# Kernel tuning notes

Measured on AMD Instinct MI355X. Metric: run time of the kernel, lower is better.

## Reference

```python
import jax, jax.numpy as jnp
import numpy as np


def setup_inputs() -> dict:
    key = jax.random.key(0)
    k1, k2, k3 = jax.random.split(key, 3)
    B, S, D, H = 64, 512, 512, 1024
    # xavier_uniform bounds
    def xavier(k, shape):
        fan_in, fan_out = shape
        limit = float(np.sqrt(6.0 / (fan_in + fan_out)))
        return jax.random.uniform(k, shape, jnp.float32, -limit, limit)
    x = jax.random.normal(k1, (B, S, D), dtype=jnp.float32)
    weight_ih = xavier(k2, (D, 4 * H))
    weight_hh = xavier(k3, (H, 4 * H))
    bias = jnp.zeros((4 * H,), dtype=jnp.float32)
    return {"x": x, "weight_ih": weight_ih, "weight_hh": weight_hh, "bias": bias}


def reference(x, weight_ih, weight_hh, bias):
    # x: (B, S, D). Faithful to the per-step loop: gates = x_t@W_ih + h@W_hh + b,
    # gate order [i, f, g, o]; zero initial states broadcast over batch.
    B = x.shape[0]
    HS = weight_hh.shape[0]
    h0 = jnp.zeros((B, HS), dtype=x.dtype)
    c0 = jnp.zeros((B, HS), dtype=x.dtype)

    def step(carry, x_t):
        h, c = carry
        gates = x_t @ weight_ih + h @ weight_hh + bias  # (B, 4*HS)
        i_t = jax.nn.sigmoid(gates[:, :HS])
        f_t = jax.nn.sigmoid(gates[:, HS:2 * HS])
        g_t = jnp.tanh(gates[:, 2 * HS:3 * HS])
        o_t = jax.nn.sigmoid(gates[:, 3 * HS:])
        c_new = f_t * c + i_t * g_t
        h_new = o_t * jnp.tanh(c_new)
        return (h_new, c_new), h_new

    xs = jnp.swapaxes(x, 0, 1)  # (S, B, D) for scan over time
    (h_t, c_t), hs = jax.lax.scan(step, (h0, c0), xs)
    hidden_seq = jnp.swapaxes(hs, 0, 1)  # (B, S, HS)
    return hidden_seq, h_t, c_t
```

## Files before the change

### kernel.cpp

```cpp
#include <hip/hip_runtime.h>
#include <hip/hip_bf16.h>

typedef __attribute__((ext_vector_type(8))) short bf16x8;
typedef __attribute__((ext_vector_type(4))) float f32x4;

constexpr int NB = 64, NS = 512, ND = 512, NH = 1024;
constexpr int G4H = 4096;
constexpr int NWG = 256, NTHR = 512;
constexpr int PS  = 20;
constexpr int TRB = 3072;

__device__ inline unsigned short f2bf(float f) {
  union { float f; unsigned u; } v; v.f = f;
  unsigned r = v.u + 0x7FFFu + ((v.u >> 16) & 1u);
  return (unsigned short)(r >> 16);
}
__device__ inline float sigmoidf_fast(float x) { return 1.0f / (1.0f + __expf(-x)); }
__device__ inline float tanhf_fast(float x) {
  float e = __expf(2.0f * x);
  return 1.0f - 2.0f / (e + 1.0f);
}
__device__ inline int swz(int row, int off) { return row * TRB + (off ^ ((row & 7) << 4)); }

__global__ void prep_kernel(const float* __restrict__ x,
                            unsigned short* __restrict__ xbf,
                            unsigned short* __restrict__ hbuf) {
  const int idx = blockIdx.x * blockDim.x + threadIdx.x;
  const int nthr = gridDim.x * blockDim.x;
  const int nh4 = NB * NH * 2 / 16;
  uint4* h4 = (uint4*)hbuf;
  for (int i = idx; i < nh4; i += nthr) h4[i] = uint4{0, 0, 0, 0};
  for (int i = idx; i < nh4; i += nthr)
    h4[nh4 + i] = uint4{0x00010001u, 0x00010001u, 0x00010001u, 0x00010001u};
  const float4* x4 = (const float4*)x;
  ushort4* xo = (ushort4*)xbf;
  const int n4 = NB * NS * ND / 4;
  for (int i = idx; i < n4; i += nthr) {
    float4 v = x4[i];
    ushort4 o;
    o.x = f2bf(v.x); o.y = f2bf(v.y); o.z = f2bf(v.z); o.w = f2bf(v.w);
    xo[i] = o;
  }
}

__global__ __launch_bounds__(NTHR)
void lstm_kernel(const float* __restrict__ Wih,
                 const float* __restrict__ Whh,
                 const float* __restrict__ bias,
                 const unsigned short* __restrict__ xbf,
                 unsigned short* __restrict__ hbuf,
                 float* __restrict__ out)
{
  const int tid  = threadIdx.x;
  const int wg   = blockIdx.x;
  const int wave = tid >> 6;
  const int lane = tid & 63;
  const int bb   = wg >> 6;
  const int hb   = wg & 63;
  const int gp   = wave & 1;
  const int q    = wave >> 1;

  __shared__ unsigned short tile[16 * 1536];
  __shared__ float part[16][16 * PS];
  __shared__ float c_state[256];

  if (tid < 256) c_state[tid] = 0.0f;

  const int kg0  = (lane >> 4) << 3;
  const int colb = (hb << 4) + (lane & 15);
  bf16x8 wx[2][4], wh[2][8];
#pragma unroll
  for (int gg = 0; gg < 2; ++gg) {
    const int col = ((gp * 2 + gg) << 10) + colb;
#pragma unroll
    for (int s = 0; s < 4; ++s) {
      const int k0 = (q * 4 + s) * 32 + kg0;
#pragma unroll
      for (int j = 0; j < 8; ++j)
        wx[gg][s][j] = (short)f2bf(Wih[(size_t)(k0 + j) * G4H + col]);
    }
#pragma unroll
    for (int u = 0; u < 8; ++u) {
      const int k0 = (q * 8 + u) * 32 + kg0;
#pragma unroll
      for (int j = 0; j < 8; ++j)
        wh[gg][u][j] = (short)f2bf(Whh[(size_t)(k0 + j) * G4H + col]);
    }
  }

  for (int c = tid; c < 1024; c += NTHR) {
    const int row = c >> 6, sl = c & 63;
    const unsigned short* src = xbf + (size_t)(bb * 16 + row) * (NS * ND) + sl * 8;
    *(uint4*)((char*)tile + swz(row, sl * 16)) = *(const uint4*)src;
  }
  for (int c = tid; c < 2048; c += NTHR) {
    const int row = c >> 7, sl = c & 127;
    *(uint4*)((char*)tile + swz(row, 1024 + sl * 16)) = uint4{0, 0, 0, 0};
  }
  __syncthreads();

  const int arow = lane & 15;
  float* ht_out = out + (size_t)NB * NS * NH;
  float* ct_out = ht_out + NB * NH;

  for (int t = 0; t < NS; ++t) {
    constexpr unsigned long long M = 0x0000000100000001ull;
    const unsigned long long T = ((t >> 1) & 1) ? M : 0ull;
    unsigned long long hq0[4], hq1[4];
    const unsigned long long* hp[4];
    if (t > 0) {
      const unsigned short* hbase = hbuf + (size_t)(t & 1) * (NB * NH);
#pragma unroll
      for (int u = 0; u < 4; ++u) {
        const int row = 2 * wave + (u >> 1);
        const int sl  = (u & 1) * 64 + lane;
        hp[u] = (const unsigned long long*)(hbase + (size_t)(bb * 16 + row) * NH + sl * 8);
        hq0[u] = __hip_atomic_load(hp[u],     __ATOMIC_RELAXED, __HIP_MEMORY_SCOPE_AGENT);
        hq1[u] = __hip_atomic_load(hp[u] + 1, __ATOMIC_RELAXED, __HIP_MEMORY_SCOPE_AGENT);
      }
    }

    f32x4 a0 = {0.f, 0.f, 0.f, 0.f}, a1 = {0.f, 0.f, 0.f, 0.f};
#pragma unroll
    for (int s = 0; s < 4; ++s) {
      const int off = ((q * 4 + s) * 32 + kg0) * 2;
      bf16x8 af = *(const bf16x8*)((const char*)tile + swz(arow, off));
      a0 = __builtin_amdgcn_mfma_f32_16x16x32_bf16(af, wx[0][s], a0, 0, 0, 0);
      a1 = __builtin_amdgcn_mfma_f32_16x16x32_bf16(af, wx[1][s], a1, 0, 0, 0);
    }

    if (t > 0) {
      while (true) {
        int stale = 0;
#pragma unroll
        for (int u = 0; u < 4; ++u)
          if ((((hq0[u] ^ T) | (hq1[u] ^ T)) & M) != 0ull) stale |= (1 << u);
        if (__all(stale == 0)) break;
#pragma unroll
        for (int u = 0; u < 4; ++u)
          if (stale & (1 << u)) {
            hq0[u] = __hip_atomic_load(hp[u],     __ATOMIC_RELAXED, __HIP_MEMORY_SCOPE_AGENT);
            hq1[u] = __hip_atomic_load(hp[u] + 1, __ATOMIC_RELAXED, __HIP_MEMORY_SCOPE_AGENT);
          }
      }
#pragma unroll
      for (int u = 0; u < 4; ++u) {
        const int row = 2 * wave + (u >> 1);
        const int sl  = (u & 1) * 64 + lane;
        uint4 v;
        v.x = (unsigned int)hq0[u];
        v.y = (unsigned int)(hq0[u] >> 32);
        v.z = (unsigned int)hq1[u];
        v.w = (unsigned int)(hq1[u] >> 32);
        *(uint4*)((char*)tile + swz(row, 1024 + sl * 16)) = v;
      }
    }
    __syncthreads();

#pragma unroll
    for (int u = 0; u < 8; ++u) {
      const int off = 1024 + ((q * 8 + u) * 32 + kg0) * 2;
      bf16x8 af = *(const bf16x8*)((const char*)tile + swz(arow, off));
      a0 = __builtin_amdgcn_mfma_f32_16x16x32_bf16(af, wh[0][u], a0, 0, 0, 0);
      a1 = __builtin_amdgcn_mfma_f32_16x16x32_bf16(af, wh[1][u], a1, 0, 0, 0);
    }

    {
      const int r0 = (lane >> 4) << 2;
      const int cc = lane & 15;
#pragma unroll
      for (int j = 0; j < 4; ++j) {
        part[wave * 2 + 0][(r0 + j) * PS + cc] = a0[j];
        part[wave * 2 + 1][(r0 + j) * PS + cc] = a1[j];
      }
    }
    __syncthreads();

    if (tid < 256) {
      const int ec = tid & 15;
      const int er = tid >> 4;
      float pre[4];
#pragma unroll
      for (int go = 0; go < 4; ++go) {
        float s = bias[(go << 10) + (hb << 4) + ec];
#pragma unroll
        for (int qq = 0; qq < 4; ++qq)
          s += part[(qq * 2 + (go >> 1)) * 2 + (go & 1)][er * PS + ec];
        pre[go] = s;
      }
      const float it = sigmoidf_fast(pre[0]);
      const float ft = sigmoidf_fast(pre[1]);
      const float gt = tanhf_fast(pre[2]);
      const float ot = sigmoidf_fast(pre[3]);
      const float cn = ft * c_state[tid] + it * gt;
      c_state[tid] = cn;
      const float hn = ot * tanhf_fast(cn);
      const int row  = bb * 16 + er;
      const int hcol = (hb << 4) + ec;
      const size_t ooff = (size_t)row * (NS * NH) + (size_t)t * NH + hcol;
      if (t == NS - 1) {
        out[ooff] = hn;
        ht_out[row * NH + hcol] = hn;
        ct_out[row * NH + hcol] = cn;
      } else {
        const unsigned int tagw = (unsigned int)(((t + 1) >> 1) & 1);
        unsigned int my  = (unsigned int)f2bf(hn);
        unsigned int pa  = (unsigned int)__shfl_xor((int)my, 1, 64);
        if ((tid & 1) == 0) {
          unsigned int myt = (my & ~1u) | tagw;
          unsigned int* p = (unsigned int*)(hbuf + (size_t)((t + 1) & 1) * (NB * NH)
                                                 + (size_t)row * NH + hcol);
          __hip_atomic_store(p, myt | (pa << 16), __ATOMIC_RELAXED, __HIP_MEMORY_SCOPE_AGENT);
        }
        __builtin_nontemporal_store(hn, &out[ooff]);
      }
    } else if (t < NS - 1) {
      for (int c = tid - 256; c < 1024; c += 256) {
        const int row = c >> 6, sl = c & 63;
        const unsigned short* src = xbf + (size_t)(bb * 16 + row) * (NS * ND)
                                        + (size_t)(t + 1) * ND + sl * 8;
        *(uint4*)((char*)tile + swz(row, sl * 16)) = *(const uint4*)src;
      }
    }
    if (t < NS - 1) __syncthreads();
  }
}

extern "C" void kernel_launch(void* const* d_in, const int* in_sizes, int n_in,
                              void* d_out, int out_size, void* d_ws, size_t ws_size,
                              hipStream_t stream) {
  const float* x    = (const float*)d_in[0];
  const float* wih  = (const float*)d_in[1];
  const float* whh  = (const float*)d_in[2];
  const float* bias = (const float*)d_in[3];
  float* out = (float*)d_out;

  unsigned short* hbuf = (unsigned short*)d_ws;
  unsigned short* xbf  = (unsigned short*)((char*)d_ws + (size_t)2 * NB * NH * 2);

  prep_kernel<<<1024, 256, 0, stream>>>(x, xbf, hbuf);

  void* args[] = { (void*)&wih, (void*)&whh, (void*)&bias,
                   (void*)&xbf, (void*)&hbuf, (void*)&out };
  hipLaunchCooperativeKernel((const void*)lstm_kernel, dim3(NWG), dim3(NTHR),
                             args, 0, stream);
}
```

Baseline: 1.358 ms.

## Double-buffer x tile and prefetch next step's input during recurrence

Splits the shared tile into a double-buffered x tile and a separate h tile. All threads now issue the global loads for the next timestep's x at the start of the step and write them into the alternate buffer before the mid-step barrier. This removes the x staging done by the upper half of the threads after the elementwise phase, and with it the trailing per-step __syncthreads. The cost is a little more LDS and more registers held live across the wait for h.

New measurement: 2.469 ms. 1.82x slower.

```diff
diff --git a/kernel.cpp b/kernel.cpp
--- a/kernel.cpp
+++ b/kernel.cpp
@@ -8,7 +8,8 @@
 constexpr int G4H = 4096;
 constexpr int NWG = 256, NTHR = 512;
 constexpr int PS  = 20;
-constexpr int TRB = 3072;
+constexpr int XRB = 1024;
+constexpr int HRB = 2048;
 
 __device__ inline unsigned short f2bf(float f) {
   union { float f; unsigned u; } v; v.f = f;
@@ -20,7 +21,8 @@
   float e = __expf(2.0f * x);
   return 1.0f - 2.0f / (e + 1.0f);
 }
-__device__ inline int swz(int row, int off) { return row * TRB + (off ^ ((row & 7) << 4)); }
+__device__ inline int swx(int row, int off) { return row * XRB + (off ^ ((row & 7) << 4)); }
+__device__ inline int swh(int row, int off) { return row * HRB + (off ^ ((row & 7) << 4)); }
 
 __global__ void prep_kernel(const float* __restrict__ x,
                             unsigned short* __restrict__ xbf,
@@ -60,7 +62,8 @@
   const int gp   = wave & 1;
   const int q    = wave >> 1;
 
-  __shared__ unsigned short tile[16 * 1536];
+  __shared__ unsigned short tile_x[2][16 * 512];
+  __shared__ unsigned short tile_h[16 * 1024];
   __shared__ float part[16][16 * PS];
   __shared__ float c_state[256];
 
@@ -88,20 +91,28 @@
     }
   }
 
+  for (int c = tid; c < 512; c += NTHR) {
+    const int row = c >> 5, sl = c & 31;
+    (void)row; (void)sl;
+    break;
+  }
   for (int c = tid; c < 1024; c += NTHR) {
     const int row = c >> 6, sl = c & 63;
     const unsigned short* src = xbf + (size_t)(bb * 16 + row) * (NS * ND) + sl * 8;
-    *(uint4*)((char*)tile + swz(row, sl * 16)) = *(const uint4*)src;
+    *(uint4*)((char*)tile_x[0] + swx(row, sl * 16)) = *(const uint4*)src;
   }
   for (int c = tid; c < 2048; c += NTHR) {
     const int row = c >> 7, sl = c & 127;
-    *(uint4*)((char*)tile + swz(row, 1024 + sl * 16)) = uint4{0, 0, 0, 0};
+    *(uint4*)((char*)tile_h + swh(row, sl * 16)) = uint4{0, 0, 0, 0};
   }
   __syncthreads();
 
   const int arow = lane & 15;
   float* ht_out = out + (size_t)NB * NS * NH;
   float* ct_out = ht_out + NB * NH;
+
+  const int sxr = tid >> 5;
+  const int sxs = (tid & 31) << 1;
 
   for (int t = 0; t < NS; ++t) {
     constexpr unsigned long long M = 0x0000000100000001ull;
@@ -119,12 +130,19 @@
         hq1[u] = __hip_atomic_load(hp[u] + 1, __ATOMIC_RELAXED, __HIP_MEMORY_SCOPE_AGENT);
       }
     }
+    uint4 xs0, xs1;
+    if (t + 1 < NS) {
+      const unsigned short* src = xbf + (size_t)(bb * 16 + sxr) * (NS * ND)
+                                      + (size_t)(t + 1) * ND + sxs * 8;
+      xs0 = *(const uint4*)src;
+      xs1 = *(const uint4*)(src + 8);
+    }
 
     f32x4 a0 = {0.f, 0.f, 0.f, 0.f}, a1 = {0.f, 0.f, 0.f, 0.f};
 #pragma unroll
     for (int s = 0; s < 4; ++s) {
       const int off = ((q * 4 + s) * 32 + kg0) * 2;
-      bf16x8 af = *(const bf16x8*)((const char*)tile + swz(arow, off));
+      bf16x8 af = *(const bf16x8*)((const char*)tile_x[t & 1] + swx(arow, off));
       a0 = __builtin_amdgcn_mfma_f32_16x16x32_bf16(af, wx[0][s], a0, 0, 0, 0);
       a1 = __builtin_amdgcn_mfma_f32_16x16x32_bf16(af, wx[1][s], a1, 0, 0, 0);
     }
@@ -152,15 +170,20 @@
         v.y = (unsigned int)(hq0[u] >> 32);
         v.z = (unsigned int)hq1[u];
         v.w = (unsigned int)(hq1[u] >> 32);
-        *(uint4*)((char*)tile + swz(row, 1024 + sl * 16)) = v;
-      }
+        *(uint4*)((char*)tile_h + swh(row, sl * 16)) = v;
+      }
+    }
+    if (t + 1 < NS) {
+      unsigned short* dst = tile_x[(t + 1) & 1];
+      *(uint4*)((char*)dst + swx(sxr, sxs * 16))       = xs0;
+      *(uint4*)((char*)dst + swx(sxr, (sxs + 1) * 16)) = xs1;
     }
     __syncthreads();
 
 #pragma unroll
     for (int u = 0; u < 8; ++u) {
-      const int off = 1024 + ((q * 8 + u) * 32 + kg0) * 2;
-      bf16x8 af = *(const bf16x8*)((const char*)tile + swz(arow, off));
+      const int off = ((q * 8 + u) * 32 + kg0) * 2;
+      bf16x8 af = *(const bf16x8*)((const char*)tile_h + swh(arow, off));
       a0 = __builtin_amdgcn_mfma_f32_16x16x32_bf16(af, wh[0][u], a0, 0, 0, 0);
       a1 = __builtin_amdgcn_mfma_f32_16x16x32_bf16(af, wh[1][u], a1, 0, 0, 0);
     }
@@ -214,15 +237,7 @@
         }
         __builtin_nontemporal_store(hn, &out[ooff]);
       }
-    } else if (t < NS - 1) {
-      for (int c = tid - 256; c < 1024; c += 256) {
-        const int row = c >> 6, sl = c & 63;
-        const unsigned short* src = xbf + (size_t)(bb * 16 + row) * (NS * ND)
-                                        + (size_t)(t + 1) * ND + sl * 8;
-        *(uint4*)((char*)tile + swz(row, sl * 16)) = *(const uint4*)src;
-      }
-    }
-    if (t < NS - 1) __syncthreads();
+    }
   }
 }
 
```
